# Kernel optimization log

Hardware: AMD Instinct MI355X
Metric: run time of the kernel (lower is better)

## Reference

```python
import jax, jax.numpy as jnp
import numpy as np

NBITS = 8
NUM_HEADS = 6


def _quant(x, alpha, nbits=NBITS):
    # LSQ-style fake quantization with straight-through estimator.
    qn = -(2 ** (nbits - 1))        # -128
    qp = 2 ** (nbits - 1) - 1       # 127
    s = jnp.clip(x / alpha, qn, qp)
    s = s + jax.lax.stop_gradient(jnp.round(s) - s)  # STE round
    return s * alpha


def setup_inputs() -> dict:
    key = jax.random.key(0)
    ks = jax.random.split(key, 12)
    B, N, C = 2, 2048, 384
    x = jax.random.normal(ks[0], (B, N, C), dtype=jnp.float32)
    w_qkv = jax.random.normal(ks[1], (3 * C, C), dtype=jnp.float32) * 0.02
    w_proj = jax.random.normal(ks[2], (C, C), dtype=jnp.float32) * 0.02
    b_proj = jnp.zeros((C,), dtype=jnp.float32)

    def alpha(k, lo, hi):
        return jax.random.uniform(k, (1,), dtype=jnp.float32, minval=lo, maxval=hi)

    return {
        "x": x,
        "w_qkv": w_qkv,
        "w_proj": w_proj,
        "b_proj": b_proj,
        "a_qkv_w": alpha(ks[3], 0.001, 0.005),
        "a_qkv_a": alpha(ks[4], 0.02, 0.05),
        "a_proj_w": alpha(ks[5], 0.001, 0.005),
        "a_proj_a": alpha(ks[6], 0.02, 0.05),
        "a_q": alpha(ks[7], 0.01, 0.03),
        "a_k": alpha(ks[8], 0.01, 0.03),
        "a_v": alpha(ks[9], 0.01, 0.03),
        "a_attn": alpha(ks[10], 0.01, 0.03),
        "a_attn2": alpha(ks[11], 0.005, 0.01),
    }


def reference(x, w_qkv, w_proj, b_proj, a_qkv_w, a_qkv_a, a_proj_w, a_proj_a,
              a_q, a_k, a_v, a_attn, a_attn2):
    B, N, C = x.shape
    H = NUM_HEADS
    D = C // H
    scale = D ** (-0.5)

    # quantized qkv linear (no bias)
    qkv = _quant(x, a_qkv_a) @ _quant(w_qkv, a_qkv_w).T          # [B,N,3C]
    qkv = qkv.reshape(B, N, 3, H, D).transpose(2, 0, 3, 1, 4)    # [3,B,H,N,D]
    q, k, v = qkv[0], qkv[1], qkv[2]
    q = _quant(q, a_q)
    k = _quant(k, a_k)
    v = _quant(v, a_v)

    attn = jnp.einsum("bhnd,bhmd->bhnm", q, k) * scale           # [B,H,N,N]
    attn = _quant(attn, a_attn)
    attn = jax.nn.softmax(attn, axis=-1)
    attn = _quant(attn, a_attn2)

    out = jnp.einsum("bhnm,bhmd->bhnd", attn, v)                 # [B,H,N,D]
    out = out.transpose(0, 2, 1, 3).reshape(B, N, C)

    # quantized output projection (with bias)
    out = _quant(out, a_proj_a) @ _quant(w_proj, a_proj_w).T + b_proj
    return out
```

## Files before the change

kernel.cpp:

```cpp
#include <hip/hip_runtime.h>
#include <math.h>


typedef int i32x4 __attribute__((ext_vector_type(4)));
typedef float f32x2 __attribute__((ext_vector_type(2)));

#define MFMA_I8(a, b, c) __builtin_amdgcn_mfma_i32_16x16x64_i8(a, b, c, 0, 0, 0)

__device__ __forceinline__ float qclip(float s) {
  return fminf(fmaxf(s, -128.0f), 127.0f);
}

__device__ __forceinline__ float fdivn(float x, float c, float rc) {
  float q0 = x * rc;
  float e = fmaf(-c, q0, x);
  return fmaf(e, rc, q0);
}

__device__ __forceinline__ f32x2 fdivn2(f32x2 x, f32x2 c, f32x2 rc) {
  f32x2 q0 = x * rc;
  f32x2 e = __builtin_elementwise_fma(-c, q0, x);
  return __builtin_elementwise_fma(e, rc, q0);
}

__device__ __forceinline__ void quant16_body(const float* __restrict__ in,
                                             signed char* __restrict__ out,
                                             float a, int i) {
  const float ra = 1.0f / a;
  const float4* p = (const float4*)in + 4 * (size_t)i;
  union { uint4 u; signed char c[16]; } o;
#pragma unroll
  for (int u = 0; u < 4; ++u) {
    float4 v = p[u];
    o.c[4 * u + 0] = (signed char)(int)rintf(qclip(fdivn(v.x, a, ra)));
    o.c[4 * u + 1] = (signed char)(int)rintf(qclip(fdivn(v.y, a, ra)));
    o.c[4 * u + 2] = (signed char)(int)rintf(qclip(fdivn(v.z, a, ra)));
    o.c[4 * u + 3] = (signed char)(int)rintf(qclip(fdivn(v.w, a, ra)));
  }
  *(uint4*)(out + 16 * (size_t)i) = o.u;
}

__global__ __launch_bounds__(256)
void prep(const float* __restrict__ x, const float* __restrict__ wqkv,
          const float* __restrict__ wproj,
          signed char* __restrict__ xq, signed char* __restrict__ wqq,
          signed char* __restrict__ wpq, float* __restrict__ E2,
          const float* __restrict__ a_qkv_a, const float* __restrict__ a_qkv_w,
          const float* __restrict__ a_proj_w, const float* __restrict__ aattn) {
  const int b = blockIdx.x, t = threadIdx.x;
  if (b < 384) {
    int i = b * 256 + t;
    if (i < 98304) quant16_body(x, xq, a_qkv_a[0], i);
  } else if (b < 492) {
    int i = (b - 384) * 256 + t;
    if (i < 27648) quant16_body(wqkv, wqq, a_qkv_w[0], i);
  } else if (b < 528) {
    int i = (b - 492) * 256 + t;
    if (i < 9216) quant16_body(wproj, wpq, a_proj_w[0], i);
  } else {
    int i = (b - 528) * 256 + t;
    float a = aattn[0];
    int vm = (i >> 8) - 128;
    int s = (i & 255) - 128;
    float m = a * (float)vm;
    E2[i] = expf(a * (float)s - m);
  }
}

__global__ __launch_bounds__(256)
void gemm_qkv(const signed char* __restrict__ A, const signed char* __restrict__ W,
              signed char* __restrict__ qws, signed char* __restrict__ kws,
              signed char* __restrict__ vwsT,
              const float* __restrict__ aa, const float* __restrict__ aw,
              const float* __restrict__ aq, const float* __restrict__ ak,
              const float* __restrict__ av) {
  __shared__ int red[2 * 64 * 33];
  const int t = threadIdx.x;
  const int w = t >> 6, lane = t & 63;
  const int lm = lane & 15, quad = lane >> 4;
  const int kw = w >> 1, nw = w & 1;
  const int m0 = blockIdx.x * 64;
  const int n0 = blockIdx.y * 64 + nw * 32;
  i32x4 acc[4][2] = {};
#pragma unroll
  for (int kk = 0; kk < 3; ++kk) {
    int k0 = kw * 192 + kk * 64;
    i32x4 af[4], bf[2];
#pragma unroll
    for (int mt = 0; mt < 4; ++mt)
      af[mt] = *(const i32x4*)(A + (size_t)(m0 + mt * 16 + lm) * 384 + k0 + quad * 16);
#pragma unroll
    for (int nt = 0; nt < 2; ++nt)
      bf[nt] = *(const i32x4*)(W + (size_t)(n0 + nt * 16 + lm) * 384 + k0 + quad * 16);
#pragma unroll
    for (int mt = 0; mt < 4; ++mt)
#pragma unroll
      for (int nt = 0; nt < 2; ++nt)
        acc[mt][nt] = MFMA_I8(af[mt], bf[nt], acc[mt][nt]);
  }
  if (kw == 1) {
    int* rw = red + nw * 2112 + lane * 33;
#pragma unroll
    for (int mt = 0; mt < 4; ++mt)
#pragma unroll
      for (int nt = 0; nt < 2; ++nt)
#pragma unroll
        for (int r = 0; r < 4; ++r)
          rw[mt * 8 + nt * 4 + r] = acc[mt][nt][r];
  }
  __syncthreads();
  if (kw == 0) {
    const int* rw = red + nw * 2112 + lane * 33;
    const float sAB = aa[0] * aw[0];
    const float vaq = aq[0], vak = ak[0], vav = av[0];
    const float rq = 1.0f / vaq, rk = 1.0f / vak, rv = 1.0f / vav;
#pragma unroll
    for (int mt = 0; mt < 4; ++mt) {
#pragma unroll
      for (int nt = 0; nt < 2; ++nt) {
        int cg = n0 + nt * 16 + lm;
        int t3 = cg / 384;
        int rem = cg - t3 * 384;
        int h = rem >> 6, d = rem & 63;
#pragma unroll
        for (int r = 0; r < 4; ++r) {
          int m = m0 + mt * 16 + quad * 4 + r;
          int bb = m >> 11, nn = m & 2047;
          int bh = bb * 6 + h;
          int sum = acc[mt][nt][r] + rw[mt * 8 + nt * 4 + r];
          float val = (float)sum * sAB;
          if (t3 == 0) {
            qws[((size_t)(bh * 2048 + nn) << 6) + d] =
                (signed char)(int)rintf(qclip(fdivn(val, vaq, rq)));
          } else if (t3 == 1) {
            kws[((size_t)(bh * 2048 + nn) << 6) + d] =
                (signed char)(int)rintf(qclip(fdivn(val, vak, rk)));
          } else {
            vwsT[((size_t)((bh << 6) + d) << 11) + nn] =
                (signed char)(int)rintf(qclip(fdivn(val, vav, rv)));
          }
        }
      }
    }
  }
}

#define TROW 2064
__global__ __launch_bounds__(256)
void attn_fused(const signed char* __restrict__ qws, const signed char* __restrict__ kws,
                const signed char* __restrict__ vwsT, const float* __restrict__ E2,
                signed char* __restrict__ ows,
                const float* __restrict__ aq, const float* __restrict__ ak,
                const float* __restrict__ aattn, const float* __restrict__ aattn2,
                const float* __restrict__ av, const float* __restrict__ apa) {
  __shared__ signed char tileS[16 * TROW];
  __shared__ float EfS[4 * 257];
  const int t = threadIdx.x;
  const int w = t >> 6, lane = t & 63;
  const int lm = lane & 15, quad = lane >> 4;
  const int i0 = blockIdx.x * 16;
  const int bh = blockIdx.y;

  const signed char* Qb = qws + ((size_t)bh << 17);
  const signed char* Kb = kws + ((size_t)bh << 17);

  i32x4 bq = *(const i32x4*)(Qb + ((size_t)(i0 + lm) << 6) + quad * 16);
  const float sc = aq[0] * ak[0] * 0.125f;
  const float ia = aattn[0];
  const float ria = 1.0f / ia;
  const f32x2 ia2v = {ia, ia}, ria2v = {ria, ria}, sc2v = {sc, sc};
#pragma unroll 4
  for (int ct = 0; ct < 32; ++ct) {
    int col0 = (w << 9) + ct * 16;
    i32x4 akf = *(const i32x4*)(Kb + ((size_t)(col0 + lm) << 6) + quad * 16);
    i32x4 z = {};
    i32x4 acc = MFMA_I8(akf, bq, z);
    f32x2 sv01 = {(float)acc[0], (float)acc[1]};
    f32x2 sv23 = {(float)acc[2], (float)acc[3]};
    f32x2 q01 = fdivn2(sv01 * sc2v, ia2v, ria2v);
    f32x2 q23 = fdivn2(sv23 * sc2v, ia2v, ria2v);
    union { unsigned int u; signed char c[4]; } pk;
    pk.c[0] = (signed char)(int)rintf(qclip(q01.x));
    pk.c[1] = (signed char)(int)rintf(qclip(q01.y));
    pk.c[2] = (signed char)(int)rintf(qclip(q23.x));
    pk.c[3] = (signed char)(int)rintf(qclip(q23.y));
    *(unsigned int*)(tileS + lm * TROW + col0 + quad * 4) = pk.u;
  }
  __syncthreads();

  const float a2 = aattn2[0];
  const float ra2 = 1.0f / a2;
  const f32x2 a22v = {a2, a2}, ra22v = {ra2, ra2};
  float* Efw = EfS + w * 257;
#pragma unroll
  for (int rr = 0; rr < 4; ++rr) {
    const int row = w * 4 + rr;
    char4* prow = (char4*)(tileS + row * TROW);
    char4 vals[8];
    int vmax = -129;
#pragma unroll
    for (int u = 0; u < 8; ++u) {
      vals[u] = prow[lane + (u << 6)];
      vmax = max(vmax, (int)vals[u].x);
      vmax = max(vmax, (int)vals[u].y);
      vmax = max(vmax, (int)vals[u].z);
      vmax = max(vmax, (int)vals[u].w);
    }
#pragma unroll
    for (int off = 32; off > 0; off >>= 1)
      vmax = max(vmax, __shfl_xor(vmax, off, 64));
#pragma unroll
    for (int u = 0; u < 4; ++u)
      Efw[u * 64 + lane] = E2[((vmax + 128) << 8) + u * 64 + lane];
    const float* Er = Efw + 128;
    float ge[8][4];
    float l = 0.0f;
#pragma unroll
    for (int u = 0; u < 8; ++u) {
      ge[u][0] = Er[(int)vals[u].x];
      ge[u][1] = Er[(int)vals[u].y];
      ge[u][2] = Er[(int)vals[u].z];
      ge[u][3] = Er[(int)vals[u].w];
      l += ge[u][0];
      l += ge[u][1];
      l += ge[u][2];
      l += ge[u][3];
    }
#pragma unroll
    for (int off = 32; off > 0; off >>= 1)
      l += __shfl_xor(l, off, 64);
    const float rl = 1.0f / l;
    const f32x2 l2v = {l, l}, rl2v = {rl, rl};
#pragma unroll
    for (int u = 0; u < 8; ++u) {
      f32x2 g01 = {ge[u][0], ge[u][1]};
      f32x2 g23 = {ge[u][2], ge[u][3]};
      f32x2 t01 = fdivn2(fdivn2(g01, l2v, rl2v), a22v, ra22v);
      f32x2 t23 = fdivn2(fdivn2(g23, l2v, rl2v), a22v, ra22v);
      union { unsigned int ui; signed char c[4]; } pk;
      pk.c[0] = (signed char)(int)rintf(qclip(t01.x));
      pk.c[1] = (signed char)(int)rintf(qclip(t01.y));
      pk.c[2] = (signed char)(int)rintf(qclip(t23.x));
      pk.c[3] = (signed char)(int)rintf(qclip(t23.y));
      *(unsigned int*)(prow + lane + (u << 6)) = pk.ui;
    }
  }
  __syncthreads();

  i32x4 areg[8];
  {
    const signed char* srow = tileS + lm * TROW + (w << 9) + quad * 16;
#pragma unroll
    for (int js = 0; js < 8; ++js)
      areg[js] = *(const i32x4*)(srow + js * 64);
  }
  const signed char* Vb = vwsT + ((size_t)bh << 17) + (w << 9);
  i32x4 acc[4] = {};
#pragma unroll
  for (int js = 0; js < 8; ++js) {
    int j0 = js * 64;
    i32x4 bf[4];
#pragma unroll
    for (int nt = 0; nt < 4; ++nt)
      bf[nt] = *(const i32x4*)(Vb + ((size_t)(nt * 16 + lm) << 11) + j0 + quad * 16);
#pragma unroll
    for (int nt = 0; nt < 4; ++nt)
      acc[nt] = MFMA_I8(areg[js], bf[nt], acc[nt]);
  }

  int* red = (int*)tileS;
  __syncthreads();
  if (w > 0) {
    int* rw = red + (w - 1) * 1088 + lane * 17;
#pragma unroll
    for (int nt = 0; nt < 4; ++nt)
#pragma unroll
      for (int r = 0; r < 4; ++r)
        rw[nt * 4 + r] = acc[nt][r];
  }
  __syncthreads();
  if (w == 0) {
    const float so = a2 * av[0];
    const float ipa = apa[0];
    const float ripa = 1.0f / ipa;
    int bb = bh / 6, h = bh % 6;
#pragma unroll
    for (int nt = 0; nt < 4; ++nt) {
      int d = nt * 16 + lm;
#pragma unroll
      for (int r = 0; r < 4; ++r) {
        int s = acc[nt][r] + red[lane * 17 + nt * 4 + r]
              + red[1088 + lane * 17 + nt * 4 + r]
              + red[2176 + lane * 17 + nt * 4 + r];
        int i = i0 + quad * 4 + r;
        ows[(size_t)((bb << 11) + i) * 384 + (h << 6) + d] =
            (signed char)(int)rintf(qclip(fdivn((float)s * so, ipa, ripa)));
      }
    }
  }
}

__global__ __launch_bounds__(256)
void gemm_proj(const signed char* __restrict__ A, const signed char* __restrict__ W,
               const float* __restrict__ bias, float* __restrict__ out,
               const float* __restrict__ apa, const float* __restrict__ apw) {
  const int t = threadIdx.x;
  const int w = t >> 6, lane = t & 63;
  const int lm = lane & 15, quad = lane >> 4;
  const int wm = w >> 1, wn = w & 1;
  const int m0 = blockIdx.x * 64 + wm * 32;
  const int n0 = blockIdx.y * 64 + wn * 32;
  i32x4 acc[2][2] = {};
  for (int k0 = 0; k0 < 384; k0 += 64) {
    i32x4 af[2], bf[2];
#pragma unroll
    for (int mt = 0; mt < 2; ++mt)
      af[mt] = *(const i32x4*)(A + (size_t)(m0 + mt * 16 + lm) * 384 + k0 + quad * 16);
#pragma unroll
    for (int nt = 0; nt < 2; ++nt)
      bf[nt] = *(const i32x4*)(W + (size_t)(n0 + nt * 16 + lm) * 384 + k0 + quad * 16);
#pragma unroll
    for (int mt = 0; mt < 2; ++mt)
#pragma unroll
      for (int nt = 0; nt < 2; ++nt)
        acc[mt][nt] = MFMA_I8(af[mt], bf[nt], acc[mt][nt]);
  }
  const float sAB = apa[0] * apw[0];
#pragma unroll
  for (int mt = 0; mt < 2; ++mt) {
#pragma unroll
    for (int nt = 0; nt < 2; ++nt) {
      int cg = n0 + nt * 16 + lm;
#pragma unroll
      for (int r = 0; r < 4; ++r) {
        int m = m0 + mt * 16 + quad * 4 + r;
        out[(size_t)m * 384 + cg] = (float)acc[mt][nt][r] * sAB + bias[cg];
      }
    }
  }
}

extern "C" void kernel_launch(void* const* d_in, const int* in_sizes, int n_in,
                              void* d_out, int out_size, void* d_ws, size_t ws_size,
                              hipStream_t stream) {
  const float* x        = (const float*)d_in[0];
  const float* w_qkv    = (const float*)d_in[1];
  const float* w_proj   = (const float*)d_in[2];
  const float* b_proj   = (const float*)d_in[3];
  const float* a_qkv_w  = (const float*)d_in[4];
  const float* a_qkv_a  = (const float*)d_in[5];
  const float* a_proj_w = (const float*)d_in[6];
  const float* a_proj_a = (const float*)d_in[7];
  const float* a_q      = (const float*)d_in[8];
  const float* a_k      = (const float*)d_in[9];
  const float* a_v      = (const float*)d_in[10];
  const float* a_attn   = (const float*)d_in[11];
  const float* a_attn2  = (const float*)d_in[12];

  char* wsb = (char*)d_ws;
  signed char* xq   = (signed char*)(wsb + 0);
  signed char* wqq  = (signed char*)(wsb + 1572864);
  signed char* wpq  = (signed char*)(wsb + 2015232);
  signed char* qws  = (signed char*)(wsb + 2162688);
  signed char* kws  = (signed char*)(wsb + 3735552);
  signed char* vwsT = (signed char*)(wsb + 5308416);
  signed char* ows  = (signed char*)(wsb + 6881280);
  float*       E2   = (float*)(wsb + 8454144);

  prep<<<784, 256, 0, stream>>>(x, w_qkv, w_proj, xq, wqq, wpq, E2,
                                a_qkv_a, a_qkv_w, a_proj_w, a_attn);
  gemm_qkv<<<dim3(64, 18), 256, 0, stream>>>(xq, wqq, qws, kws, vwsT,
                                             a_qkv_a, a_qkv_w, a_q, a_k, a_v);
  attn_fused<<<dim3(128, 12), 256, 0, stream>>>(qws, kws, vwsT, E2, ows,
                                                a_q, a_k, a_attn, a_attn2,
                                                a_v, a_proj_a);
  gemm_proj<<<dim3(64, 6), 256, 0, stream>>>(ows, wpq, b_proj, (float*)d_out,
                                             a_proj_a, a_proj_w);
}
```

Baseline: 153.4 us.

## Split-K the output projection GEMM across waves with LDS reduction; use fmed3 clip

The projection GEMM now splits K=384 into two halves handled by different wave pairs. Each wave covers a 64x32 tile and the two halves are summed through shared memory before the epilogue. This gives more independent MFMAs per wave and a shorter serial K loop, at the cost of LDS traffic, a block barrier, and half the waves going idle in the epilogue. The clip helper also switches to a single med3 instruction.

```diff
diff --git a/kernel.cpp b/kernel.cpp
--- a/kernel.cpp
+++ b/kernel.cpp
@@ -8,7 +8,7 @@
 #define MFMA_I8(a, b, c) __builtin_amdgcn_mfma_i32_16x16x64_i8(a, b, c, 0, 0, 0)
 
 __device__ __forceinline__ float qclip(float s) {
-  return fminf(fmaxf(s, -128.0f), 127.0f);
+  return __builtin_amdgcn_fmed3f(s, -128.0f, 127.0f);
 }
 
 __device__ __forceinline__ float fdivn(float x, float c, float rc) {
@@ -304,37 +304,55 @@
 void gemm_proj(const signed char* __restrict__ A, const signed char* __restrict__ W,
                const float* __restrict__ bias, float* __restrict__ out,
                const float* __restrict__ apa, const float* __restrict__ apw) {
+  __shared__ int red[2 * 64 * 33];
   const int t = threadIdx.x;
   const int w = t >> 6, lane = t & 63;
   const int lm = lane & 15, quad = lane >> 4;
-  const int wm = w >> 1, wn = w & 1;
-  const int m0 = blockIdx.x * 64 + wm * 32;
-  const int n0 = blockIdx.y * 64 + wn * 32;
-  i32x4 acc[2][2] = {};
-  for (int k0 = 0; k0 < 384; k0 += 64) {
-    i32x4 af[2], bf[2];
-#pragma unroll
-    for (int mt = 0; mt < 2; ++mt)
+  const int kw = w >> 1, nw = w & 1;
+  const int m0 = blockIdx.x * 64;
+  const int n0 = blockIdx.y * 64 + nw * 32;
+  i32x4 acc[4][2] = {};
+#pragma unroll
+  for (int kk = 0; kk < 3; ++kk) {
+    int k0 = kw * 192 + kk * 64;
+    i32x4 af[4], bf[2];
+#pragma unroll
+    for (int mt = 0; mt < 4; ++mt)
       af[mt] = *(const i32x4*)(A + (size_t)(m0 + mt * 16 + lm) * 384 + k0 + quad * 16);
 #pragma unroll
     for (int nt = 0; nt < 2; ++nt)
       bf[nt] = *(const i32x4*)(W + (size_t)(n0 + nt * 16 + lm) * 384 + k0 + quad * 16);
 #pragma unroll
-    for (int mt = 0; mt < 2; ++mt)
+    for (int mt = 0; mt < 4; ++mt)
 #pragma unroll
       for (int nt = 0; nt < 2; ++nt)
         acc[mt][nt] = MFMA_I8(af[mt], bf[nt], acc[mt][nt]);
   }
-  const float sAB = apa[0] * apw[0];
-#pragma unroll
-  for (int mt = 0; mt < 2; ++mt) {
-#pragma unroll
-    for (int nt = 0; nt < 2; ++nt) {
-      int cg = n0 + nt * 16 + lm;
-#pragma unroll
-      for (int r = 0; r < 4; ++r) {
-        int m = m0 + mt * 16 + quad * 4 + r;
-        out[(size_t)m * 384 + cg] = (float)acc[mt][nt][r] * sAB + bias[cg];
+  if (kw == 1) {
+    int* rw = red + nw * 2112 + lane * 33;
+#pragma unroll
+    for (int mt = 0; mt < 4; ++mt)
+#pragma unroll
+      for (int nt = 0; nt < 2; ++nt)
+#pragma unroll
+        for (int r = 0; r < 4; ++r)
+          rw[mt * 8 + nt * 4 + r] = acc[mt][nt][r];
+  }
+  __syncthreads();
+  if (kw == 0) {
+    const int* rw = red + nw * 2112 + lane * 33;
+    const float sAB = apa[0] * apw[0];
+#pragma unroll
+    for (int mt = 0; mt < 4; ++mt) {
+#pragma unroll
+      for (int nt = 0; nt < 2; ++nt) {
+        int cg = n0 + nt * 16 + lm;
+#pragma unroll
+        for (int r = 0; r < 4; ++r) {
+          int m = m0 + mt * 16 + quad * 4 + r;
+          int sum = acc[mt][nt][r] + rw[mt * 8 + nt * 4 + r];
+          out[(size_t)m * 384 + cg] = (float)sum * sAB + bias[cg];
+        }
       }
     }
   }
```

Result: no change. 152.3 us (median of 2 runs) (-0.7%).
